# Kernel tuning notes

Hardware: AMD Instinct MI355X
Metric: run time of the kernel (lower is better)

Reference implementation:

```python
import jax, jax.numpy as jnp
import numpy as np

NUM_HEADS = 16
ROPE_THETA = 10000.0
SEQ = 2048
D_MODEL = 2048


def _rope(x):
    # x: (seq, heads, head_dim). Equinox RotaryPositionalEmbedding:
    # rotate_half variant with tiled (non-interleaved) cos/sin.
    S, H, hd = x.shape
    half = hd // 2
    freqs = 1.0 / (ROPE_THETA ** (jnp.arange(0, half, dtype=jnp.float32) * 2.0 / hd))  # (half,)
    t = jnp.arange(S, dtype=jnp.float32)
    angles = jnp.outer(t, freqs)  # (S, half)
    cos = jnp.tile(jnp.cos(angles), (1, 2))[:, None, :]  # (S, 1, hd)
    sin = jnp.tile(jnp.sin(angles), (1, 2))[:, None, :]
    x1, x2 = jnp.split(x, 2, axis=-1)
    rot = jnp.concatenate((-x2, x1), axis=-1)  # rotate_half
    return (x * cos + rot * sin).astype(x.dtype)


def setup_inputs() -> dict:
    key = jax.random.key(0)
    ks = jax.random.split(key, 7)
    mk = lambda k, scale=1.0: (jax.random.normal(k, (SEQ, D_MODEL), dtype=jnp.float32) * scale)
    return {
        "query": mk(ks[0]),
        "key_": mk(ks[1]),
        "value": mk(ks[2]),
        "Wq": jax.random.normal(ks[3], (D_MODEL, D_MODEL), dtype=jnp.float32) / np.sqrt(D_MODEL),
        "Wk": jax.random.normal(ks[4], (D_MODEL, D_MODEL), dtype=jnp.float32) / np.sqrt(D_MODEL),
        "Wv": jax.random.normal(ks[5], (D_MODEL, D_MODEL), dtype=jnp.float32) / np.sqrt(D_MODEL),
        "Wo": jax.random.normal(ks[6], (D_MODEL, D_MODEL), dtype=jnp.float32) / np.sqrt(D_MODEL),
    }


def reference(query, key_, value, Wq, Wk, Wv, Wo):
    S, D = query.shape
    H = NUM_HEADS
    hd = D // H
    # QKV projections (equinox Linear: y = W @ x, vmapped over seq -> x @ W.T)
    q = (query @ Wq.T).reshape(S, H, hd)
    k = (key_ @ Wk.T).reshape(S, H, hd)
    v = (value @ Wv.T).reshape(S, H, hd)
    # Per-head RoPE on q and k
    q = _rope(q)
    k = _rope(k)
    # Causal attention, scale 1/sqrt(head_dim) (dropout_p=0, inference)
    attn = jax.nn.dot_product_attention(q[None], k[None], v[None], is_causal=True)[0]  # (S, H, hd)
    # Output projection
    return attn.reshape(S, D) @ Wo.T
```

## Files before the change

### kernel.cpp

```cpp
#include <hip/hip_runtime.h>

typedef unsigned short u16;
typedef __attribute__((ext_vector_type(8))) __bf16 bf16x8;
typedef __attribute__((ext_vector_type(4))) float f32x4;

#define D_MODEL 2048
#define SEQ 2048
#define NHEAD 16
#define HDIM 128

#define AS1 __attribute__((address_space(1)))
#define AS3 __attribute__((address_space(3)))
#define GL2LDS(g, l) __builtin_amdgcn_global_load_lds((AS1 const void*)(g), (AS3 void*)(l), 16, 0, 0)

__device__ __forceinline__ u16 f2bf(float f) {
  unsigned u = __float_as_uint(f);
  u += 0x7fff + ((u >> 16) & 1);
  return (u16)(u >> 16);
}
__device__ __forceinline__ float bf2f(u16 h) {
  return __uint_as_float(((unsigned)h) << 16);
}
__device__ __forceinline__ float fexp2(float x) {
#if __has_builtin(__builtin_amdgcn_exp2f)
  return __builtin_amdgcn_exp2f(x);
#else
  return __expf(x * 0.69314718055994531f);
#endif
}

__global__ __launch_bounds__(256) void k_cast7(const float* i0, const float* i1, const float* i2,
                                               const float* i3, const float* i4, const float* i5,
                                               const float* i6,
                                               u16* o0, u16* o1, u16* o2, u16* o3, u16* o4,
                                               u16* o5, u16* o6) {
  const float* in; u16* out;
  switch (blockIdx.y) {
    case 0: in = i0; out = o0; break;
    case 1: in = i1; out = o1; break;
    case 2: in = i2; out = o2; break;
    case 3: in = i3; out = o3; break;
    case 4: in = i4; out = o4; break;
    case 5: in = i5; out = o5; break;
    default: in = i6; out = o6; break;
  }
  const int i = blockIdx.x * blockDim.x + threadIdx.x;
  const float4 v = reinterpret_cast<const float4*>(in)[i];
  ushort4 o;
  o.x = f2bf(v.x); o.y = f2bf(v.y); o.z = f2bf(v.z); o.w = f2bf(v.w);
  reinterpret_cast<ushort4*>(out)[i] = o;
}

__device__ __forceinline__ void gemm_nt_body(const u16* __restrict__ A, const u16* __restrict__ B,
                                             void* __restrict__ C, u16* As, u16* Bs, int outmode) {
  const int tn = blockIdx.x, tm = blockIdx.y;
  const int t = threadIdx.x;
  const int lane = t & 63, w = t >> 6;
  const int wr = w >> 1, wc = w & 1;
  const int lrow = lane & 15, lk = (lane >> 4) * 8;
  f32x4 acc[4][4] = {};
  for (int kt = 0; kt < D_MODEL; kt += 64) {
#pragma unroll
    for (int c = 0; c < 4; ++c) {
      const int elem = c * 2048 + t * 8;
      const int r = elem >> 6, col = elem & 63;
      GL2LDS(A + (size_t)(tm * 128 + r) * D_MODEL + kt + col, As + c * 2048 + w * 512);
      GL2LDS(B + (size_t)(tn * 128 + r) * D_MODEL + kt + col, Bs + c * 2048 + w * 512);
    }
    __syncthreads();
#pragma unroll
    for (int kk = 0; kk < 2; ++kk) {
      bf16x8 af[4], bfr[4];
#pragma unroll
      for (int i = 0; i < 4; ++i) {
        af[i]  = *(const bf16x8*)(As + (wr * 64 + i * 16 + lrow) * 64 + kk * 32 + lk);
        bfr[i] = *(const bf16x8*)(Bs + (wc * 64 + i * 16 + lrow) * 64 + kk * 32 + lk);
      }
#pragma unroll
      for (int i = 0; i < 4; ++i)
#pragma unroll
        for (int j = 0; j < 4; ++j)
          acc[i][j] = __builtin_amdgcn_mfma_f32_16x16x32_bf16(af[i], bfr[j], acc[i][j], 0, 0, 0);
    }
    __syncthreads();
  }
  const int crow0 = tm * 128 + wr * 64 + (lane >> 4) * 4;
  const int ccol0 = tn * 128 + wc * 64 + lrow;
  if (outmode == 2) {
#pragma unroll
    for (int i = 0; i < 4; ++i)
#pragma unroll
      for (int j = 0; j < 4; ++j) {
        ushort4 o;
        o.x = f2bf(acc[i][j][0]); o.y = f2bf(acc[i][j][1]);
        o.z = f2bf(acc[i][j][2]); o.w = f2bf(acc[i][j][3]);
        *(ushort4*)((u16*)C + (size_t)(ccol0 + j * 16) * D_MODEL + crow0 + i * 16) = o;
      }
  } else {
#pragma unroll
    for (int i = 0; i < 4; ++i)
#pragma unroll
      for (int j = 0; j < 4; ++j)
#pragma unroll
        for (int r = 0; r < 4; ++r)
          ((u16*)C)[(size_t)(crow0 + i * 16 + r) * D_MODEL + ccol0 + j * 16] = f2bf(acc[i][j][r]);
  }
}

__global__ __launch_bounds__(256) void k_gemm_qkv(const u16* Xq, const u16* Xk, const u16* Xv,
                                                  const u16* Wq, const u16* Wk, const u16* Wv,
                                                  u16* Q, u16* K, u16* VT) {
  __shared__ u16 As[128 * 64], Bs[128 * 64];
  const int z = blockIdx.z;
  const u16* A = (z == 0) ? Xq : (z == 1) ? Xk : Xv;
  const u16* B = (z == 0) ? Wq : (z == 1) ? Wk : Wv;
  u16* C = (z == 0) ? Q : (z == 1) ? K : VT;
  gemm_nt_body(A, B, C, As, Bs, (z == 2) ? 2 : 0);
}

__global__ __launch_bounds__(256) void k_gemm_out(const u16* __restrict__ A, const u16* __restrict__ B,
                                                  float* __restrict__ C) {
  __shared__ u16 As[128 * 64], Bs[64 * 64];
  const int tn = blockIdx.x, tm = blockIdx.y;
  const int t = threadIdx.x;
  const int lane = t & 63, w = t >> 6;
  const int wr = w >> 1, wc = w & 1;
  const int lrow = lane & 15, lk = (lane >> 4) * 8;
  f32x4 acc[4][2] = {};
  for (int kt = 0; kt < D_MODEL; kt += 64) {
#pragma unroll
    for (int c = 0; c < 4; ++c) {
      const int elem = c * 2048 + t * 8;
      const int r = elem >> 6, col = elem & 63;
      GL2LDS(A + (size_t)(tm * 128 + r) * D_MODEL + kt + col, As + c * 2048 + w * 512);
    }
#pragma unroll
    for (int c = 0; c < 2; ++c) {
      const int elem = c * 2048 + t * 8;
      const int r = elem >> 6, col = elem & 63;
      GL2LDS(B + (size_t)(tn * 64 + r) * D_MODEL + kt + col, Bs + c * 2048 + w * 512);
    }
    __syncthreads();
#pragma unroll
    for (int kk = 0; kk < 2; ++kk) {
      bf16x8 af[4], bfr[2];
#pragma unroll
      for (int i = 0; i < 4; ++i)
        af[i]  = *(const bf16x8*)(As + (wr * 64 + i * 16 + lrow) * 64 + kk * 32 + lk);
#pragma unroll
      for (int j = 0; j < 2; ++j)
        bfr[j] = *(const bf16x8*)(Bs + (wc * 32 + j * 16 + lrow) * 64 + kk * 32 + lk);
#pragma unroll
      for (int i = 0; i < 4; ++i)
#pragma unroll
        for (int j = 0; j < 2; ++j)
          acc[i][j] = __builtin_amdgcn_mfma_f32_16x16x32_bf16(af[i], bfr[j], acc[i][j], 0, 0, 0);
    }
    __syncthreads();
  }
  const int crow0 = tm * 128 + wr * 64 + (lane >> 4) * 4;
  const int ccol0 = tn * 64 + wc * 32 + lrow;
#pragma unroll
  for (int i = 0; i < 4; ++i)
#pragma unroll
    for (int j = 0; j < 2; ++j)
#pragma unroll
      for (int r = 0; r < 4; ++r)
        C[(size_t)(crow0 + i * 16 + r) * D_MODEL + ccol0 + j * 16] = acc[i][j][r];
}

__global__ __launch_bounds__(256) void k_rope(u16* Q, u16* K) {
  const int idx = blockIdx.x * blockDim.x + threadIdx.x;
  u16* X = blockIdx.y ? K : Q;
  const float scale = blockIdx.y ? 1.0f : (1.4426950408889634f * 0.08838834764831845f);
  const int s = idx >> 10;
  const int h = (idx >> 6) & 15;
  const int j = idx & 63;
  const float freq = __expf((float)j * -0.14391156831212787f);
  float sn, cs;
  sincosf((float)s * freq, &sn, &cs);
  const size_t base = (size_t)s * D_MODEL + h * HDIM + j;
  const float x1 = bf2f(X[base]), x2 = bf2f(X[base + 64]);
  X[base]      = f2bf((x1 * cs - x2 * sn) * scale);
  X[base + 64] = f2bf((x2 * cs + x1 * sn) * scale);
}

__global__ __launch_bounds__(256, 2) void k_attn(const u16* __restrict__ Q, const u16* __restrict__ K,
                                                 const u16* __restrict__ VT, u16* __restrict__ O) {
  __shared__ u16 Kb[2][64 * 128];
  __shared__ u16 Vb[2][128 * 64];
  __shared__ u16 Pl[4][32 * 64];
  const int bx = blockIdx.x;
  const int h = bx & 15;
  const int qt = 31 - (bx >> 4);
  const int t = threadIdx.x;
  const int lane = t & 63, w = t >> 6;
  const int mh = w & 1, par = w >> 1;
  const int lrow = lane & 15, g = lane >> 4, lk = g * 8;
  const int qrow0 = qt * 64 + mh * 32;

  bf16x8 qf[2][4];
#pragma unroll
  for (int mi = 0; mi < 2; ++mi)
#pragma unroll
    for (int ks = 0; ks < 4; ++ks)
      qf[mi][ks] = *(const bf16x8*)(Q + (size_t)(qrow0 + mi * 16 + lrow) * D_MODEL + h * HDIM + ks * 32 + lk);

  f32x4 accO[2][8] = {};
  float m_run[2][4], l_run[2][4];
#pragma unroll
  for (int mi = 0; mi < 2; ++mi)
#pragma unroll
    for (int r = 0; r < 4; ++r) { m_run[mi][r] = -1e30f; l_run[mi][r] = 0.f; }

  const int nt = qt + 1;
  const int nss = (nt + 1) >> 1;
#pragma unroll 1
  for (int s = 0; s < nss; ++s) {
    const int t0 = 2 * s;
    const int t1 = (2 * s + 1 < nt) ? 2 * s + 1 : nt - 1;
#pragma unroll
    for (int i = 0; i < 4; ++i) {
      const int rk = w * 16 + i * 4 + (lane >> 4);
      const int ck = lane & 15;
      GL2LDS(K + (size_t)(t0 * 64 + rk) * D_MODEL + h * HDIM + ((ck ^ (rk & 15)) * 8),
             Kb[0] + (w * 16 + i * 4) * 128);
      GL2LDS(K + (size_t)(t1 * 64 + rk) * D_MODEL + h * HDIM + ((ck ^ (rk & 15)) * 8),
             Kb[1] + (w * 16 + i * 4) * 128);
      const int rv = w * 32 + i * 8 + (lane >> 3);
      const int cv = lane & 7;
      GL2LDS(VT + (size_t)(h * HDIM + rv) * D_MODEL + t0 * 64 + ((cv ^ (rv & 7)) * 8),
             Vb[0] + (w * 32 + i * 8) * 64);
      GL2LDS(VT + (size_t)(h * HDIM + rv) * D_MODEL + t1 * 64 + ((cv ^ (rv & 7)) * 8),
             Vb[1] + (w * 32 + i * 8) * 64);
    }
    __syncthreads();

    const int T = 2 * s + par;
    if (T < nt) {
      f32x4 sc[2][4] = {};
#pragma unroll
      for (int ks = 0; ks < 4; ++ks) {
        bf16x8 kf[4];
#pragma unroll
        for (int ni = 0; ni < 4; ++ni)
          kf[ni] = *(const bf16x8*)(&Kb[par][(ni * 16 + lrow) * 128 + ((ks * 4 + g) ^ lrow) * 8]);
#pragma unroll
        for (int mi = 0; mi < 2; ++mi)
#pragma unroll
          for (int ni = 0; ni < 4; ++ni)
            sc[mi][ni] = __builtin_amdgcn_mfma_f32_16x16x32_bf16(qf[mi][ks], kf[ni], sc[mi][ni], 0, 0, 0);
      }

      if (T == qt) {
        const int kv = T * 64;
#pragma unroll
        for (int mi = 0; mi < 2; ++mi)
#pragma unroll
          for (int ni = 0; ni < 4; ++ni) {
            const int colg = kv + ni * 16 + lrow;
#pragma unroll
            for (int r = 0; r < 4; ++r) {
              const int rowg = qrow0 + mi * 16 + g * 4 + r;
              if (colg > rowg) sc[mi][ni][r] = -1e30f;
            }
          }
      }

#pragma unroll
      for (int mi = 0; mi < 2; ++mi)
#pragma unroll
        for (int r = 0; r < 4; ++r) {
          float pm = fmaxf(fmaxf(sc[mi][0][r], sc[mi][1][r]), fmaxf(sc[mi][2][r], sc[mi][3][r]));
          pm = fmaxf(pm, __shfl_xor(pm, 1));
          pm = fmaxf(pm, __shfl_xor(pm, 2));
          pm = fmaxf(pm, __shfl_xor(pm, 4));
          pm = fmaxf(pm, __shfl_xor(pm, 8));
          const float mo = m_run[mi][r];
          const float mn = fmaxf(mo, pm);
          const float sf = fexp2(mo - mn);
          float rs = 0.f;
#pragma unroll
          for (int ni = 0; ni < 4; ++ni) {
            const float p = fexp2(sc[mi][ni][r] - mn);
            sc[mi][ni][r] = p;
            rs += p;
          }
          rs += __shfl_xor(rs, 1);
          rs += __shfl_xor(rs, 2);
          rs += __shfl_xor(rs, 4);
          rs += __shfl_xor(rs, 8);
          l_run[mi][r] = l_run[mi][r] * sf + rs;
          m_run[mi][r] = mn;
#pragma unroll
          for (int dt = 0; dt < 8; ++dt) accO[mi][dt][r] *= sf;
        }

#pragma unroll
      for (int mi = 0; mi < 2; ++mi)
#pragma unroll
        for (int ni = 0; ni < 4; ++ni)
#pragma unroll
          for (int r = 0; r < 4; ++r) {
            const int row = mi * 16 + g * 4 + r;
            const int chnk = (2 * ni + (lrow >> 3)) ^ (row & 7);
            Pl[w][row * 64 + chnk * 8 + (lrow & 7)] = f2bf(sc[mi][ni][r]);
          }
      asm volatile("s_waitcnt lgkmcnt(0)" ::: "memory");

#pragma unroll
      for (int ks2 = 0; ks2 < 2; ++ks2) {
        bf16x8 pf[2];
#pragma unroll
        for (int mi = 0; mi < 2; ++mi) {
          const int row = mi * 16 + lrow;
          pf[mi] = *(const bf16x8*)(&Pl[w][row * 64 + ((ks2 * 4 + g) ^ (row & 7)) * 8]);
        }
#pragma unroll
        for (int dt = 0; dt < 8; ++dt) {
          const int R = dt * 16 + lrow;
          const bf16x8 vf = *(const bf16x8*)(&Vb[par][R * 64 + ((ks2 * 4 + g) ^ (R & 7)) * 8]);
#pragma unroll
          for (int mi = 0; mi < 2; ++mi)
            accO[mi][dt] = __builtin_amdgcn_mfma_f32_16x16x32_bf16(pf[mi], vf, accO[mi][dt], 0, 0, 0);
        }
      }
    }
    __syncthreads();
  }

  float* mrg = (float*)&Kb[0][0];
  float* mlb = (float*)&Vb[0][0];
  if (par == 1) {
#pragma unroll
    for (int mi = 0; mi < 2; ++mi)
#pragma unroll
      for (int dt = 0; dt < 8; ++dt)
#pragma unroll
        for (int r = 0; r < 4; ++r)
          mrg[mh * 4096 + (mi * 16 + g * 4 + r) * 128 + dt * 16 + lrow] = accO[mi][dt][r];
#pragma unroll
    for (int mi = 0; mi < 2; ++mi)
#pragma unroll
      for (int r = 0; r < 4; ++r) {
        const int row = mi * 16 + g * 4 + r;
        mlb[mh * 64 + row * 2]     = m_run[mi][r];
        mlb[mh * 64 + row * 2 + 1] = l_run[mi][r];
      }
  }
  __syncthreads();
  if (par == 0) {
#pragma unroll
    for (int mi = 0; mi < 2; ++mi)
#pragma unroll
      for (int r = 0; r < 4; ++r) {
        const int row = mi * 16 + g * 4 + r;
        const float m1 = mlb[mh * 64 + row * 2];
        const float l1 = mlb[mh * 64 + row * 2 + 1];
        const float mn = fmaxf(m_run[mi][r], m1);
        const float f0 = fexp2(m_run[mi][r] - mn);
        const float f1 = fexp2(m1 - mn);
        const float inv = 1.0f / (l_run[mi][r] * f0 + l1 * f1);
        const size_t grow = (size_t)(qrow0 + row);
#pragma unroll
        for (int dt = 0; dt < 8; ++dt) {
          const float v1 = mrg[mh * 4096 + row * 128 + dt * 16 + lrow];
          O[grow * D_MODEL + h * HDIM + dt * 16 + lrow] =
              f2bf((accO[mi][dt][r] * f0 + v1 * f1) * inv);
        }
      }
  }
}

extern "C" void kernel_launch(void* const* d_in, const int* in_sizes, int n_in,
                              void* d_out, int out_size, void* d_ws, size_t ws_size,
                              hipStream_t stream) {
  const float* query = (const float*)d_in[0];
  const float* key_  = (const float*)d_in[1];
  const float* value = (const float*)d_in[2];
  const float* Wq    = (const float*)d_in[3];
  const float* Wk    = (const float*)d_in[4];
  const float* Wv    = (const float*)d_in[5];
  const float* Wo    = (const float*)d_in[6];
  float* out = (float*)d_out;

  const size_t TS = (size_t)SEQ * D_MODEL;
  u16* ws  = (u16*)d_ws;
  u16* bXq = ws + 0 * TS;
  u16* bXk = ws + 1 * TS;
  u16* bXv = ws + 2 * TS;
  u16* bWq = ws + 3 * TS;
  u16* bWk = ws + 4 * TS;
  u16* bWv = ws + 5 * TS;
  u16* bWo = ws + 6 * TS;
  u16* bQ  = ws + 7 * TS;
  u16* bK  = ws + 8 * TS;
  u16* bVT = ws + 9 * TS;
  u16* bA  = ws + 10 * TS;

  const int n4 = (int)(TS / 4);
  k_cast7<<<dim3(n4 / 256, 7), 256, 0, stream>>>(query, key_, value, Wq, Wk, Wv, Wo,
                                                 bXq, bXk, bXv, bWq, bWk, bWv, bWo);

  k_gemm_qkv<<<dim3(16, 16, 3), 256, 0, stream>>>(bXq, bXk, bXv, bWq, bWk, bWv, bQ, bK, bVT);

  k_rope<<<dim3((SEQ * NHEAD * 64) / 256, 2), 256, 0, stream>>>(bQ, bK);

  k_attn<<<dim3(512), 256, 0, stream>>>(bQ, bK, bVT, bA);

  k_gemm_out<<<dim3(32, 16), 256, 0, stream>>>(bA, bWo, out);
}
```

Before: 351.4 us.

## Double-buffer GEMM LDS tiles and XOR-swizzle layout to avoid bank conflicts

```diff
diff --git a/kernel.cpp b/kernel.cpp
--- a/kernel.cpp
+++ b/kernel.cpp
@@ -51,30 +51,54 @@
   reinterpret_cast<ushort4*>(out)[i] = o;
 }
 
+__device__ __forceinline__ void stage128(const u16* __restrict__ P, u16* dst, int row0, int kt,
+                                         int t, int w) {
+#pragma unroll
+  for (int c = 0; c < 4; ++c) {
+    const int r = (c * 2048 + t * 8) >> 6;
+    const int ch = ((t & 7) ^ (r & 7)) * 8;
+    GL2LDS(P + (size_t)(row0 + r) * D_MODEL + kt + ch, dst + c * 2048 + w * 512);
+  }
+}
+__device__ __forceinline__ void stage64(const u16* __restrict__ P, u16* dst, int row0, int kt,
+                                        int t, int w) {
+#pragma unroll
+  for (int c = 0; c < 2; ++c) {
+    const int r = (c * 2048 + t * 8) >> 6;
+    const int ch = ((t & 7) ^ (r & 7)) * 8;
+    GL2LDS(P + (size_t)(row0 + r) * D_MODEL + kt + ch, dst + c * 2048 + w * 512);
+  }
+}
+
 __device__ __forceinline__ void gemm_nt_body(const u16* __restrict__ A, const u16* __restrict__ B,
-                                             void* __restrict__ C, u16* As, u16* Bs, int outmode) {
+                                             void* __restrict__ C, u16* As0, u16* As1,
+                                             u16* Bs0, u16* Bs1, int outmode) {
   const int tn = blockIdx.x, tm = blockIdx.y;
   const int t = threadIdx.x;
   const int lane = t & 63, w = t >> 6;
   const int wr = w >> 1, wc = w & 1;
-  const int lrow = lane & 15, lk = (lane >> 4) * 8;
+  const int lrow = lane & 15, g = lane >> 4;
   f32x4 acc[4][4] = {};
+
+  stage128(A, As0, tm * 128, 0, t, w);
+  stage128(B, Bs0, tn * 128, 0, t, w);
+  __syncthreads();
+
+  u16 *Ar = As0, *Br = Bs0, *Aw = As1, *Bw = Bs1;
+#pragma unroll 1
   for (int kt = 0; kt < D_MODEL; kt += 64) {
-#pragma unroll
-    for (int c = 0; c < 4; ++c) {
-      const int elem = c * 2048 + t * 8;
-      const int r = elem >> 6, col = elem & 63;
-      GL2LDS(A + (size_t)(tm * 128 + r) * D_MODEL + kt + col, As + c * 2048 + w * 512);
-      GL2LDS(B + (size_t)(tn * 128 + r) * D_MODEL + kt + col, Bs + c * 2048 + w * 512);
-    }
-    __syncthreads();
+    if (kt + 64 < D_MODEL) {
+      stage128(A, Aw, tm * 128, kt + 64, t, w);
+      stage128(B, Bw, tn * 128, kt + 64, t, w);
+    }
 #pragma unroll
     for (int kk = 0; kk < 2; ++kk) {
       bf16x8 af[4], bfr[4];
 #pragma unroll
       for (int i = 0; i < 4; ++i) {
-        af[i]  = *(const bf16x8*)(As + (wr * 64 + i * 16 + lrow) * 64 + kk * 32 + lk);
-        bfr[i] = *(const bf16x8*)(Bs + (wc * 64 + i * 16 + lrow) * 64 + kk * 32 + lk);
+        const int sw = (((kk << 2) + g) ^ (lrow & 7)) * 8;
+        af[i]  = *(const bf16x8*)(Ar + (wr * 64 + i * 16 + lrow) * 64 + sw);
+        bfr[i] = *(const bf16x8*)(Br + (wc * 64 + i * 16 + lrow) * 64 + sw);
       }
 #pragma unroll
       for (int i = 0; i < 4; ++i)
@@ -83,7 +107,11 @@
           acc[i][j] = __builtin_amdgcn_mfma_f32_16x16x32_bf16(af[i], bfr[j], acc[i][j], 0, 0, 0);
     }
     __syncthreads();
-  }
+    u16* tp;
+    tp = Ar; Ar = Aw; Aw = tp;
+    tp = Br; Br = Bw; Bw = tp;
+  }
+
   const int crow0 = tm * 128 + wr * 64 + (lane >> 4) * 4;
   const int ccol0 = tn * 128 + wc * 64 + lrow;
   if (outmode == 2) {
@@ -107,49 +135,47 @@
   }
 }
 
-__global__ __launch_bounds__(256) void k_gemm_qkv(const u16* Xq, const u16* Xk, const u16* Xv,
-                                                  const u16* Wq, const u16* Wk, const u16* Wv,
-                                                  u16* Q, u16* K, u16* VT) {
-  __shared__ u16 As[128 * 64], Bs[128 * 64];
+__global__ __launch_bounds__(256, 2) void k_gemm_qkv(const u16* Xq, const u16* Xk, const u16* Xv,
+                                                     const u16* Wq, const u16* Wk, const u16* Wv,
+                                                     u16* Q, u16* K, u16* VT) {
+  __shared__ u16 As[2][128 * 64], Bs[2][128 * 64];
   const int z = blockIdx.z;
   const u16* A = (z == 0) ? Xq : (z == 1) ? Xk : Xv;
   const u16* B = (z == 0) ? Wq : (z == 1) ? Wk : Wv;
   u16* C = (z == 0) ? Q : (z == 1) ? K : VT;
-  gemm_nt_body(A, B, C, As, Bs, (z == 2) ? 2 : 0);
-}
-
-__global__ __launch_bounds__(256) void k_gemm_out(const u16* __restrict__ A, const u16* __restrict__ B,
-                                                  float* __restrict__ C) {
-  __shared__ u16 As[128 * 64], Bs[64 * 64];
+  gemm_nt_body(A, B, C, As[0], As[1], Bs[0], Bs[1], (z == 2) ? 2 : 0);
+}
+
+__global__ __launch_bounds__(256, 2) void k_gemm_out(const u16* __restrict__ A, const u16* __restrict__ B,
+                                                     float* __restrict__ C) {
+  __shared__ u16 As[2][128 * 64], Bs[2][64 * 64];
   const int tn = blockIdx.x, tm = blockIdx.y;
   const int t = threadIdx.x;
   const int lane = t & 63, w = t >> 6;
   const int wr = w >> 1, wc = w & 1;
-  const int lrow = lane & 15, lk = (lane >> 4) * 8;
+  const int lrow = lane & 15, g = lane >> 4;
   f32x4 acc[4][2] = {};
+
+  stage128(A, As[0], tm * 128, 0, t, w);
+  stage64(B, Bs[0], tn * 64, 0, t, w);
+  __syncthreads();
+
+  u16 *Ar = As[0], *Br = Bs[0], *Aw = As[1], *Bw = Bs[1];
+#pragma unroll 1
   for (int kt = 0; kt < D_MODEL; kt += 64) {
-#pragma unroll
-    for (int c = 0; c < 4; ++c) {
-      const int elem = c * 2048 + t * 8;
-      const int r = elem >> 6, col = elem & 63;
-      GL2LDS(A + (size_t)(tm * 128 + r) * D_MODEL + kt + col, As + c * 2048 + w * 512);
-    }
-#pragma unroll
-    for (int c = 0; c < 2; ++c) {
-      const int elem = c * 2048 + t * 8;
-      const int r = elem >> 6, col = elem & 63;
-      GL2LDS(B + (size_t)(tn * 64 + r) * D_MODEL + kt + col, Bs + c * 2048 + w * 512);
-    }
-    __syncthreads();
+    if (kt + 64 < D_MODEL) {
+      stage128(A, Aw, tm * 128, kt + 64, t, w);
+      stage64(B, Bw, tn * 64, kt + 64, t, w);
+    }
 #pragma unroll
     for (int kk = 0; kk < 2; ++kk) {
       bf16x8 af[4], bfr[2];
 #pragma unroll
-      for (int i = 0; i < 4; ++i)
-        af[i]  = *(const bf16x8*)(As + (wr * 64 + i * 16 + lrow) * 64 + kk * 32 + lk);
-#pragma unroll
-      for (int j = 0; j < 2; ++j)
-        bfr[j] = *(const bf16x8*)(Bs + (wc * 32 + j * 16 + lrow) * 64 + kk * 32 + lk);
+      for (int i = 0; i < 4; ++i) {
+        const int sw = (((kk << 2) + g) ^ (lrow & 7)) * 8;
+        af[i] = *(const bf16x8*)(Ar + (wr * 64 + i * 16 + lrow) * 64 + sw);
+        if (i < 2) bfr[i] = *(const bf16x8*)(Br + (wc * 32 + i * 16 + lrow) * 64 + sw);
+      }
 #pragma unroll
       for (int i = 0; i < 4; ++i)
 #pragma unroll
@@ -157,6 +183,9 @@
           acc[i][j] = __builtin_amdgcn_mfma_f32_16x16x32_bf16(af[i], bfr[j], acc[i][j], 0, 0, 0);
     }
     __syncthreads();
+    u16* tp;
+    tp = Ar; Ar = Aw; Aw = tp;
+    tp = Br; Br = Bw; Bw = tp;
   }
   const int crow0 = tm * 128 + wr * 64 + (lane >> 4) * 4;
   const int ccol0 = tn * 64 + wc * 32 + lrow;
```

New measurement: 310.2 us. 1.13x faster.
